# Kernel tuning notes

Hardware: AMD Instinct MI355X
Metric: run time of the kernel (lower is better)

## Reference

```python
import jax, jax.numpy as jnp
import numpy as np

FP8_E4M3_MAX = 448.0
BLOCK_SIZE = 128


def _block_quant_dequant_e4m3(x, block_size=BLOCK_SIZE):
    """Per-block (along last dim) FP8 E4M3 fake quantize: returns dequantized fp32."""
    M, K = x.shape
    nb = K // block_size
    xb = x.reshape(M, nb, block_size)
    amax = jnp.clip(jnp.max(jnp.abs(xb), axis=-1, keepdims=True), 1e-12, None)
    scale = FP8_E4M3_MAX / amax  # per-block scale, [M, nb, 1]
    q = jnp.clip(xb * scale, -FP8_E4M3_MAX, FP8_E4M3_MAX).astype(jnp.float8_e4m3fn)
    deq = q.astype(jnp.float32) / scale
    return deq.reshape(M, K)


def _dual_quantize_weight(w, block_size=BLOCK_SIZE):
    """TCFP-12 dual quantization: FP8 hi component + FP8-quantized residual (lo)."""
    w_hi = _block_quant_dequant_e4m3(w, block_size)
    residual = w - w_hi
    w_lo = _block_quant_dequant_e4m3(residual, block_size)
    return w_hi + w_lo


def setup_inputs() -> dict:
    key = jax.random.key(0)
    k1, k2, k3 = jax.random.split(key, 3)
    B, T, DIN, DOUT = 8, 4096, 1024, 1024
    x = jax.random.normal(k1, (B, T, DIN), dtype=jnp.float32)
    weight = jax.random.normal(k2, (DOUT, DIN), dtype=jnp.float32) * 0.02
    bias = jax.random.normal(k3, (DOUT,), dtype=jnp.float32) * 0.01
    return {"x": x, "weight": weight, "bias": bias}


def reference(x, weight, bias):
    # Block-quantize activations (fake-quant, per 128-col block, E4M3)
    B, T, DIN = x.shape
    x2d = x.reshape(-1, DIN)
    x_q = _block_quant_dequant_e4m3(x2d, BLOCK_SIZE)
    # Dual-quantize weight: hi + residual lo components
    w_q = _dual_quantize_weight(weight, BLOCK_SIZE)
    # Block-scaled GEMM (dequantized reference math) + bias
    out2d = x_q @ w_q.T + bias
    return out2d.reshape(B, T, -1)
```

## Files before the change

### kernel.cpp

```cpp
#include <hip/hip_runtime.h>
#include <hip/hip_bf16.h>

typedef __bf16 bf16x8 __attribute__((ext_vector_type(8)));
typedef float  f32x4  __attribute__((ext_vector_type(4)));

#define GLOAD_LDS16(gptr, lptr)                                                  \
  __builtin_amdgcn_global_load_lds(                                              \
      (const __attribute__((address_space(1))) void*)(gptr),                     \
      (__attribute__((address_space(3))) void*)(lptr), 16, 0, 0)

__device__ __forceinline__ unsigned short f2bf(float f) {
  __hip_bfloat16 h = __float2bfloat16(f);
  return __builtin_bit_cast(unsigned short, h);
}

__device__ __forceinline__ void fq32(float* __restrict__ v) {
  float am = 0.0f;
#pragma unroll
  for (int i = 0; i < 32; ++i) am = fmaxf(am, fabsf(v[i]));
  am = fmaxf(am, __shfl_xor(am, 1));
  am = fmaxf(am, __shfl_xor(am, 2));
  am = fmaxf(am, 1e-12f);
  const float scale = 448.0f / am;
  const float inv   = am * (1.0f / 448.0f);
#pragma unroll
  for (int i = 0; i < 32; i += 4) {
    float c0 = fminf(fmaxf(v[i + 0] * scale, -448.0f), 448.0f);
    float c1 = fminf(fmaxf(v[i + 1] * scale, -448.0f), 448.0f);
    float c2 = fminf(fmaxf(v[i + 2] * scale, -448.0f), 448.0f);
    float c3 = fminf(fmaxf(v[i + 3] * scale, -448.0f), 448.0f);
    int pk = __builtin_amdgcn_cvt_pk_fp8_f32(c0, c1, 0, false);
    pk = __builtin_amdgcn_cvt_pk_fp8_f32(c2, c3, pk, true);
    v[i + 0] = __builtin_amdgcn_cvt_f32_fp8(pk, 0) * inv;
    v[i + 1] = __builtin_amdgcn_cvt_f32_fp8(pk, 1) * inv;
    v[i + 2] = __builtin_amdgcn_cvt_f32_fp8(pk, 2) * inv;
    v[i + 3] = __builtin_amdgcn_cvt_f32_fp8(pk, 3) * inv;
  }
}

__global__ __launch_bounds__(256) void quant_x_k(const float* __restrict__ x,
                                                 unsigned short* __restrict__ xq) {
  const size_t wave  = ((size_t)blockIdx.x * 256 + threadIdx.x) >> 6;
  const int    lane  = threadIdx.x & 63;
  const size_t qbase = wave * 2048 + (size_t)(lane >> 2) * 128 + (lane & 3) * 4;
  float v[32];
#pragma unroll
  for (int i = 0; i < 8; ++i)
    *(float4*)&v[i * 4] = *(const float4*)(x + qbase + i * 16);
  fq32(v);
#pragma unroll
  for (int i = 0; i < 8; ++i) {
    union { uint2 u; unsigned short s[4]; } pk;
#pragma unroll
    for (int e = 0; e < 4; ++e) pk.s[e] = f2bf(v[i * 4 + e]);
    *(uint2*)(xq + qbase + i * 16) = pk.u;
  }
}

__global__ __launch_bounds__(256) void quant_w_k(const float* __restrict__ w,
                                                 unsigned short* __restrict__ wq) {
  const size_t wave  = ((size_t)blockIdx.x * 256 + threadIdx.x) >> 6;
  const int    lane  = threadIdx.x & 63;
  const size_t qbase = wave * 2048 + (size_t)(lane >> 2) * 128 + (lane & 3) * 4;
  float a[32], h[32], r[32];
#pragma unroll
  for (int i = 0; i < 8; ++i)
    *(float4*)&a[i * 4] = *(const float4*)(w + qbase + i * 16);
#pragma unroll
  for (int i = 0; i < 32; ++i) h[i] = a[i];
  fq32(h);
#pragma unroll
  for (int i = 0; i < 32; ++i) r[i] = a[i] - h[i];
  fq32(r);
#pragma unroll
  for (int i = 0; i < 8; ++i) {
    union { uint2 u; unsigned short s[4]; } pk;
#pragma unroll
    for (int e = 0; e < 4; ++e) pk.s[e] = f2bf(h[i * 4 + e] + r[i * 4 + e]);
    *(uint2*)(wq + qbase + i * 16) = pk.u;
  }
}

#define BM 256
#define BN 256
#define BK 64

#define VM4()  asm volatile("s_waitcnt vmcnt(4)" ::: "memory")
#define VM2()  asm volatile("s_waitcnt vmcnt(2)" ::: "memory")
#define VM0()  asm volatile("s_waitcnt vmcnt(0)" ::: "memory")
#define LG0()  do { asm volatile("s_waitcnt lgkmcnt(0)" ::: "memory");           \
                    __builtin_amdgcn_sched_barrier(0); } while (0)
#define BAR()  __builtin_amdgcn_s_barrier()

__global__ __launch_bounds__(512, 2) void gemm_bt_bias(
    const unsigned short* __restrict__ A,
    const unsigned short* __restrict__ B,
    const float* __restrict__ bias,
    float* __restrict__ C,
    int M, int N, int K) {
  __shared__ unsigned short lds[65536];
  unsigned short* ldsA = lds;
  unsigned short* ldsB = lds + 32768;

  const int tid  = threadIdx.x;
  const int wv   = tid >> 6;
  const int lane = tid & 63;
  const int nbn  = N / BN;
  const int nbm  = M / BM;

  int bm, bn;
  if ((nbm & 7) == 0) {
    const int xcd = blockIdx.x & 7;
    const int j   = blockIdx.x >> 3;
    bn = j % nbn;
    bm = xcd * (nbm >> 3) + j / nbn;
  } else {
    bn = blockIdx.x % nbn;
    bm = blockIdx.x / nbn;
  }

  const int wr = wv >> 2;
  const int wc = wv & 3;

  f32x4  acc[8][4] = {};
  bf16x8 a[4][2], b01[2][2], b23[2][2];

  const int    srcChunk = ((lane & 7) ^ ((lane >> 3) & 7)) * 8;
  const size_t laneSrc  = (size_t)(lane >> 3) * K + srcChunk;
  const unsigned short* gA = A + (size_t)bm * BM * K + laneSrc;
  const unsigned short* gB = B + (size_t)bn * BN * K + laneSrc;
  const int lr0 = wv * 16, lr1 = wv * 16 + 8;
  auto arow = [](int mq, int lr) { return mq * 64 + (lr < 64 ? lr : 64 + lr); };
  auto brow = [](int v,  int lr) { return v * 32 + (lr >> 5) * 64 + (lr & 31); };
  const int rA[2][2] = {{arow(0, lr0), arow(0, lr1)}, {arow(1, lr0), arow(1, lr1)}};
  const int rB[2][2] = {{brow(0, lr0), brow(0, lr1)}, {brow(1, lr0), brow(1, lr1)}};

  auto stageA = [&](int buf, int mq, int kt) {
#pragma unroll
    for (int t = 0; t < 2; ++t) {
      const int rb = rA[mq][t];
      GLOAD_LDS16(gA + (size_t)rb * K + kt * BK,
                  ldsA + buf * 16384 + rb * 64 + lane * 8);
    }
  };
  auto stageB = [&](int buf, int v, int kt) {
#pragma unroll
    for (int t = 0; t < 2; ++t) {
      const int rb = rB[v][t];
      GLOAD_LDS16(gB + (size_t)rb * K + kt * BK,
                  ldsB + buf * 16384 + rb * 64 + lane * 8);
    }
  };

  const int fRow = lane & 15;
  const int q4   = lane >> 4;
  const int s8   = fRow & 7;
  const int sw0  = ((q4)     ^ s8) * 8;
  const int sw1  = ((4 + q4) ^ s8) * 8;
  const int aRO  = (wr * 128 + fRow) * 64;
  const int bRO  = (wc * 64  + fRow) * 64;

  auto dsA = [&](int buf, int mq) {
    const unsigned short* p = ldsA + buf * 16384 + aRO + mq * 4096;
#pragma unroll
    for (int m = 0; m < 4; ++m) {
      a[m][0] = *(const bf16x8*)(p + m * 1024 + sw0);
      a[m][1] = *(const bf16x8*)(p + m * 1024 + sw1);
    }
  };
  auto dsB = [&](int buf, int njp, bf16x8 (&bb)[2][2]) {
    const unsigned short* p = ldsB + buf * 16384 + bRO + njp * 2048;
#pragma unroll
    for (int n = 0; n < 2; ++n) {
      bb[n][0] = *(const bf16x8*)(p + n * 1024 + sw0);
      bb[n][1] = *(const bf16x8*)(p + n * 1024 + sw1);
    }
  };

  auto mm = [&](int mq, int njp, bf16x8 (&bb)[2][2]) {
    __builtin_amdgcn_s_setprio(1);
#pragma unroll
    for (int m = 0; m < 4; ++m)
#pragma unroll
      for (int n = 0; n < 2; ++n)
#pragma unroll
        for (int k = 0; k < 2; ++k)
          acc[mq * 4 + m][njp * 2 + n] = __builtin_amdgcn_mfma_f32_16x16x32_bf16(
              a[m][k], bb[n][k], acc[mq * 4 + m][njp * 2 + n], 0, 0, 0);
    __builtin_amdgcn_s_setprio(0);
  };

  stageA(0, 0, 0); stageB(0, 0, 0); stageB(0, 1, 0); stageA(0, 1, 0);
  VM4(); BAR();

  const int niter = K / (2 * BK);
  for (int i = 0; i < niter - 1; ++i) {
    const int t1 = 2 * i + 1, t2 = 2 * i + 2;
    dsA(0, 0); dsB(0, 0, b01); stageA(1, 0, t1);
    BAR(); LG0(); mm(0, 0, b01); VM4(); BAR();
    dsB(0, 1, b23); stageB(1, 0, t1);
    BAR(); LG0(); mm(0, 1, b23); VM4(); BAR();
    dsA(0, 1); stageB(1, 1, t1);
    BAR(); LG0(); mm(1, 0, b01); BAR();
    stageA(1, 1, t1);
    BAR(); mm(1, 1, b23); VM4(); BAR();
    dsA(1, 0); dsB(1, 0, b01); stageA(0, 0, t2);
    BAR(); LG0(); mm(0, 0, b01); VM4(); BAR();
    dsB(1, 1, b23); stageB(0, 0, t2);
    BAR(); LG0(); mm(0, 1, b23); VM4(); BAR();
    dsA(1, 1); stageB(0, 1, t2);
    BAR(); LG0(); mm(1, 0, b01); BAR();
    stageA(0, 1, t2);
    BAR(); mm(1, 1, b23); VM4(); BAR();
  }
  {
    const int t1 = 2 * niter - 1;
    dsA(0, 0); dsB(0, 0, b01); stageA(1, 0, t1);
    BAR(); LG0(); mm(0, 0, b01); VM4(); BAR();
    dsB(0, 1, b23); stageB(1, 0, t1);
    BAR(); LG0(); mm(0, 1, b23); VM4(); BAR();
    dsA(0, 1); stageB(1, 1, t1);
    BAR(); LG0(); mm(1, 0, b01); BAR();
    stageA(1, 1, t1);
    BAR(); mm(1, 1, b23); VM4(); BAR();
    dsA(1, 0); dsB(1, 0, b01);
    BAR(); LG0(); mm(0, 0, b01); VM2(); BAR();
    dsB(1, 1, b23);
    BAR(); LG0(); mm(0, 1, b23); VM0(); BAR();
    dsA(1, 1);
    BAR(); LG0(); mm(1, 0, b01); BAR();
    mm(1, 1, b23);
  }

  const int    n0 = bn * BN + wc * 64 + fRow;
  const size_t m0 = (size_t)bm * BM + wr * 128 + (q4 << 2);
#pragma unroll
  for (int nj = 0; nj < 4; ++nj) {
    const int col = n0 + nj * 16;
    const float bv = bias[col];
#pragma unroll
    for (int mi = 0; mi < 8; ++mi) {
      const size_t base = (m0 + (size_t)mi * 16) * N + col;
#pragma unroll
      for (int r = 0; r < 4; ++r)
        C[base + (size_t)r * N] = acc[mi][nj][r] + bv;
    }
  }
}

extern "C" void kernel_launch(void* const* d_in, const int* in_sizes, int n_in,
                              void* d_out, int out_size, void* d_ws, size_t ws_size,
                              hipStream_t stream) {
  const float* x    = (const float*)d_in[0];
  const float* w    = (const float*)d_in[1];
  const float* bias = (const float*)d_in[2];

  const int DOUT = in_sizes[2];
  const int DIN  = in_sizes[1] / DOUT;
  const int M    = in_sizes[0] / DIN;

  unsigned short* xq = (unsigned short*)d_ws;
  unsigned short* wq = xq + (size_t)M * DIN;

  hipLaunchKernelGGL(quant_x_k, dim3((size_t)M * DIN / 32 / 256), dim3(256), 0,
                     stream, x, xq);
  hipLaunchKernelGGL(quant_w_k, dim3((size_t)DOUT * DIN / 32 / 256), dim3(256), 0,
                     stream, w, wq);

  const int grid = (M / BM) * (DOUT / BN);
  hipLaunchKernelGGL(gemm_bt_bias, dim3(grid), dim3(512), 0, stream,
                     xq, wq, bias, (float*)d_out, M, DOUT, DIN);
}
```

Measured before the change: 316.0 us.

## Shrink GEMM block to 256x128 with 4 waves and single-buffered in-place LDS staging

Changes the GEMM tile from 256x256 with 8 waves to 256x128 with 4 waves, and drops the double-buffered LDS in favour of a single buffer. Each quarter of the tile is refilled as soon as it has been read into registers, with adjusted vmcnt waits. LDS use drops to 48KB per block, so more blocks can be resident per CU. In exchange, B operands are reused less across M, global traffic for A rises, and the in-place overwrite pipeline may expose more latency.

```diff
diff --git a/kernel.cpp b/kernel.cpp
--- a/kernel.cpp
+++ b/kernel.cpp
@@ -82,25 +82,23 @@
 }
 
 #define BM 256
-#define BN 256
+#define BN 128
 #define BK 64
 
-#define VM4()  asm volatile("s_waitcnt vmcnt(4)" ::: "memory")
-#define VM2()  asm volatile("s_waitcnt vmcnt(2)" ::: "memory")
-#define VM0()  asm volatile("s_waitcnt vmcnt(0)" ::: "memory")
+#define VMG(n) asm volatile("s_waitcnt vmcnt(" #n ")" ::: "memory")
 #define LG0()  do { asm volatile("s_waitcnt lgkmcnt(0)" ::: "memory");           \
                     __builtin_amdgcn_sched_barrier(0); } while (0)
+#define SB0()  __builtin_amdgcn_sched_barrier(0)
 #define BAR()  __builtin_amdgcn_s_barrier()
 
-__global__ __launch_bounds__(512, 2) void gemm_bt_bias(
+__global__ __launch_bounds__(256, 2) void gemm_bt_bias(
     const unsigned short* __restrict__ A,
     const unsigned short* __restrict__ B,
     const float* __restrict__ bias,
     float* __restrict__ C,
     int M, int N, int K) {
-  __shared__ unsigned short lds[65536];
-  unsigned short* ldsA = lds;
-  unsigned short* ldsB = lds + 32768;
+  __shared__ unsigned short ldsA[BM * BK];
+  __shared__ unsigned short ldsB[BN * BK];
 
   const int tid  = threadIdx.x;
   const int wv   = tid >> 6;
@@ -119,8 +117,8 @@
     bm = blockIdx.x / nbn;
   }
 
-  const int wr = wv >> 2;
-  const int wc = wv & 3;
+  const int wr = wv >> 1;
+  const int wc = wv & 1;
 
   f32x4  acc[8][4] = {};
   bf16x8 a[4][2], b01[2][2], b23[2][2];
@@ -129,26 +127,31 @@
   const size_t laneSrc  = (size_t)(lane >> 3) * K + srcChunk;
   const unsigned short* gA = A + (size_t)bm * BM * K + laneSrc;
   const unsigned short* gB = B + (size_t)bn * BN * K + laneSrc;
-  const int lr0 = wv * 16, lr1 = wv * 16 + 8;
-  auto arow = [](int mq, int lr) { return mq * 64 + (lr < 64 ? lr : 64 + lr); };
-  auto brow = [](int v,  int lr) { return v * 32 + (lr >> 5) * 64 + (lr & 31); };
-  const int rA[2][2] = {{arow(0, lr0), arow(0, lr1)}, {arow(1, lr0), arow(1, lr1)}};
-  const int rB[2][2] = {{brow(0, lr0), brow(0, lr1)}, {brow(1, lr0), brow(1, lr1)}};
-
-  auto stageA = [&](int buf, int mq, int kt) {
+
+  int rU0[4], rV0[2];
+#pragma unroll
+  for (int t = 0; t < 4; ++t) {
+    const int g = wv * 32 + t * 8;
+    rU0[t] = (g < 64) ? g : g + 64;
+  }
+#pragma unroll
+  for (int t = 0; t < 2; ++t) {
+    const int g = wv * 16 + t * 8;
+    rV0[t] = ((g >> 5) << 6) + (g & 31);
+  }
+
+  auto stageA = [&](int mq, int kt) {
+#pragma unroll
+    for (int t = 0; t < 4; ++t) {
+      const int rb = rU0[t] + mq * 64;
+      GLOAD_LDS16(gA + (size_t)rb * K + kt * BK, ldsA + rb * 64 + lane * 8);
+    }
+  };
+  auto stageB = [&](int v, int kt) {
 #pragma unroll
     for (int t = 0; t < 2; ++t) {
-      const int rb = rA[mq][t];
-      GLOAD_LDS16(gA + (size_t)rb * K + kt * BK,
-                  ldsA + buf * 16384 + rb * 64 + lane * 8);
-    }
-  };
-  auto stageB = [&](int buf, int v, int kt) {
-#pragma unroll
-    for (int t = 0; t < 2; ++t) {
-      const int rb = rB[v][t];
-      GLOAD_LDS16(gB + (size_t)rb * K + kt * BK,
-                  ldsB + buf * 16384 + rb * 64 + lane * 8);
+      const int rb = rV0[t] + v * 32;
+      GLOAD_LDS16(gB + (size_t)rb * K + kt * BK, ldsB + rb * 64 + lane * 8);
     }
   };
 
@@ -160,16 +163,16 @@
   const int aRO  = (wr * 128 + fRow) * 64;
   const int bRO  = (wc * 64  + fRow) * 64;
 
-  auto dsA = [&](int buf, int mq) {
-    const unsigned short* p = ldsA + buf * 16384 + aRO + mq * 4096;
+  auto dsA = [&](int mq) {
+    const unsigned short* p = ldsA + aRO + mq * 4096;
 #pragma unroll
     for (int m = 0; m < 4; ++m) {
       a[m][0] = *(const bf16x8*)(p + m * 1024 + sw0);
       a[m][1] = *(const bf16x8*)(p + m * 1024 + sw1);
     }
   };
-  auto dsB = [&](int buf, int njp, bf16x8 (&bb)[2][2]) {
-    const unsigned short* p = ldsB + buf * 16384 + bRO + njp * 2048;
+  auto dsB = [&](int njp, bf16x8 (&bb)[2][2]) {
+    const unsigned short* p = ldsB + bRO + njp * 2048;
 #pragma unroll
     for (int n = 0; n < 2; ++n) {
       bb[n][0] = *(const bf16x8*)(p + n * 1024 + sw0);
@@ -190,44 +193,26 @@
     __builtin_amdgcn_s_setprio(0);
   };
 
-  stageA(0, 0, 0); stageB(0, 0, 0); stageB(0, 1, 0); stageA(0, 1, 0);
-  VM4(); BAR();
-
-  const int niter = K / (2 * BK);
-  for (int i = 0; i < niter - 1; ++i) {
-    const int t1 = 2 * i + 1, t2 = 2 * i + 2;
-    dsA(0, 0); dsB(0, 0, b01); stageA(1, 0, t1);
-    BAR(); LG0(); mm(0, 0, b01); VM4(); BAR();
-    dsB(0, 1, b23); stageB(1, 0, t1);
-    BAR(); LG0(); mm(0, 1, b23); VM4(); BAR();
-    dsA(0, 1); stageB(1, 1, t1);
+  stageA(0, 0); SB0(); stageB(0, 0); SB0(); stageB(1, 0); SB0(); stageA(1, 0);
+  VMG(6); BAR();
+
+  const int ntile = K / BK;
+  for (int t = 0; t < ntile - 1; ++t) {
+    dsA(0); dsB(0, b01);
+    BAR(); LG0(); mm(0, 0, b01); VMG(4); BAR();
+    dsB(1, b23); stageA(0, t + 1);
+    BAR(); LG0(); mm(0, 1, b23); VMG(4); BAR();
+    dsA(1); stageB(0, t + 1);
     BAR(); LG0(); mm(1, 0, b01); BAR();
-    stageA(1, 1, t1);
-    BAR(); mm(1, 1, b23); VM4(); BAR();
-    dsA(1, 0); dsB(1, 0, b01); stageA(0, 0, t2);
-    BAR(); LG0(); mm(0, 0, b01); VM4(); BAR();
-    dsB(1, 1, b23); stageB(0, 0, t2);
-    BAR(); LG0(); mm(0, 1, b23); VM4(); BAR();
-    dsA(1, 1); stageB(0, 1, t2);
-    BAR(); LG0(); mm(1, 0, b01); BAR();
-    stageA(0, 1, t2);
-    BAR(); mm(1, 1, b23); VM4(); BAR();
+    stageB(1, t + 1); SB0(); stageA(1, t + 1);
+    BAR(); mm(1, 1, b23); VMG(6); BAR();
   }
   {
-    const int t1 = 2 * niter - 1;
-    dsA(0, 0); dsB(0, 0, b01); stageA(1, 0, t1);
-    BAR(); LG0(); mm(0, 0, b01); VM4(); BAR();
-    dsB(0, 1, b23); stageB(1, 0, t1);
-    BAR(); LG0(); mm(0, 1, b23); VM4(); BAR();
-    dsA(0, 1); stageB(1, 1, t1);
-    BAR(); LG0(); mm(1, 0, b01); BAR();
-    stageA(1, 1, t1);
-    BAR(); mm(1, 1, b23); VM4(); BAR();
-    dsA(1, 0); dsB(1, 0, b01);
-    BAR(); LG0(); mm(0, 0, b01); VM2(); BAR();
-    dsB(1, 1, b23);
-    BAR(); LG0(); mm(0, 1, b23); VM0(); BAR();
-    dsA(1, 1);
+    dsA(0); dsB(0, b01);
+    BAR(); LG0(); mm(0, 0, b01); VMG(4); BAR();
+    dsB(1, b23);
+    BAR(); LG0(); mm(0, 1, b23); VMG(0); BAR();
+    dsA(1);
     BAR(); LG0(); mm(1, 0, b01); BAR();
     mm(1, 1, b23);
   }
@@ -268,6 +253,6 @@
                      stream, w, wq);
 
   const int grid = (M / BM) * (DOUT / BN);
-  hipLaunchKernelGGL(gemm_bt_bias, dim3(grid), dim3(512), 0, stream,
+  hipLaunchKernelGGL(gemm_bt_bias, dim3(grid), dim3(256), 0, stream,
                      xq, wq, bias, (float*)d_out, M, DOUT, DIN);
 }
```

New measurement: 310.8 us. Within noise of the previous version (-1.6%).
